# Optimization experiments

Measured on AMD Instinct MI355X. Metric: run time of the kernel, lower is better.

## Reference

```python
import jax, jax.numpy as jnp
import numpy as np

N = 15872   # number of predictions (31 * 512)
D = 129     # 128 image features + 1 objectness score
H = 128     # block MLP hidden width
IN = 2 * D + 1  # neighbor feats + main feats + add_info (IoU)
NUM_BLOCKS = 2


def _lin(k, fi, fo):
    return jax.random.normal(k, (fi, fo), jnp.float32) / np.sqrt(fi).astype(np.float32)


def setup_inputs() -> dict:
    key = jax.random.key(0)
    ks = jax.random.split(key, 24)
    # ragged neighborhood structure: mean size 16, exactly E = 16*N edges
    sizes = (np.arange(N) % 31) + 1
    E = int(sizes.sum())  # 253952
    rng = np.random.default_rng(0)
    nbr_idx = rng.integers(0, N, size=E).astype(np.int32)
    self_idx = np.repeat(np.arange(N, dtype=np.int32), sizes)  # sorted segment ids

    inp = {
        "interpolated": jax.random.normal(ks[0], (N, D), jnp.float32),
        "add_info": jax.random.uniform(ks[1], (E, 1), dtype=jnp.float32),
        "neighborhood_sizes": jnp.asarray(sizes, jnp.int32),
        "neighborhoods_indexes": jnp.asarray(nbr_idx),
        "self_indexes": jnp.asarray(self_idx),
    }
    # two (block, output) model pairs
    inp["b0_W1"] = _lin(ks[2], IN, H); inp["b0_b1"] = jnp.zeros((H,), jnp.float32)
    inp["b0_W2"] = _lin(ks[3], H, H);  inp["b0_b2"] = jnp.zeros((H,), jnp.float32)
    inp["b0_Wo"] = _lin(ks[4], H, D); inp["b0_bo"] = jnp.zeros((D,), jnp.float32)
    inp["b1_W1"] = _lin(ks[5], IN, H); inp["b1_b1"] = jnp.zeros((H,), jnp.float32)
    inp["b1_W2"] = _lin(ks[6], H, H);  inp["b1_b2"] = jnp.zeros((H,), jnp.float32)
    inp["b1_Wo"] = _lin(ks[7], H, D); inp["b1_bo"] = jnp.zeros((D,), jnp.float32)
    # final layers: 129 -> 64 -> 1
    inp["f_W1"] = _lin(ks[8], D, 64); inp["f_b1"] = jnp.zeros((64,), jnp.float32)
    inp["f_W2"] = _lin(ks[9], 64, 1); inp["f_b2"] = jnp.zeros((1,), jnp.float32)
    return inp


def _lnms_forward(interpolated, add_info, params, nbr_idx, self_idx):
    # params: list of (W1, b1, W2, b2, Wo, bo) per block, plus (fW1, fb1, fW2, fb2)
    for (W1, b1, W2, b2, Wo, bo) in params[:-1]:
        nbr = interpolated[nbr_idx]    # (E, D) gather of neighbor representations
        main = interpolated[self_idx]  # (E, D) gather of owning prediction
        x = jnp.concatenate([nbr, main, add_info], axis=1)  # (E, 2D+1)
        h = jax.nn.relu(x @ W1 + b1)
        h = jax.nn.relu(h @ W2 + b2)   # (E, H) processed neighborhoods
        # ragged per-neighborhood max pool (segments are contiguous/sorted)
        pooled = jax.ops.segment_max(h, self_idx, num_segments=N,
                                     indices_are_sorted=True)  # (N, H)
        block_output = pooled @ Wo + bo  # (N, D)
        interpolated = interpolated + block_output  # residual scatter-update
    fW1, fb1, fW2, fb2 = params[-1]
    return jax.nn.relu(interpolated @ fW1 + fb1) @ fW2 + fb2  # (N, 1)


def reference(interpolated, add_info,
              b0_W1, b0_b1, b0_W2, b0_b2, b0_Wo, b0_bo,
              b1_W1, b1_b1, b1_W2, b1_b2, b1_Wo, b1_bo,
              f_W1, f_b1, f_W2, f_b2,
              neighborhood_sizes, neighborhoods_indexes, self_indexes):
    params = [
        (b0_W1, b0_b1, b0_W2, b0_b2, b0_Wo, b0_bo),
        (b1_W1, b1_b1, b1_W2, b1_b2, b1_Wo, b1_bo),
        (f_W1, f_b1, f_W2, f_b2),
    ]
    return _lnms_forward(interpolated, add_info, params,
                         neighborhoods_indexes, self_indexes)
```

## Files before the change

### kernel.cpp

```cpp
#include <hip/hip_runtime.h>

#define NSEG 15872
#define DD 129
#define HH 128
#define NTILE (NSEG / 16)

typedef __attribute__((ext_vector_type(8))) short s16x8;
typedef __attribute__((ext_vector_type(4))) short s16x4;
typedef __attribute__((ext_vector_type(4))) float f32x4;
typedef __attribute__((ext_vector_type(16))) float f32x16;

__device__ __forceinline__ unsigned short f2bf(float x) {
  union { float f; unsigned u; } c; c.f = x;
  unsigned r = c.u + 0x7FFFu + ((c.u >> 16) & 1u);
  return (unsigned short)(r >> 16);
}
__device__ __forceinline__ float bf2f(unsigned short v) {
  union { unsigned u; float f; } c; c.u = ((unsigned)v) << 16; return c.f;
}

__global__ __launch_bounds__(256) void scan_sort_kernel(
    const int* __restrict__ sizes, int* __restrict__ offs,
    int* __restrict__ sorted) {
  extern __shared__ int dynS[];
  int* szS = dynS;
  int* tmpS = dynS + NSEG;
  __shared__ int sums[256];
  __shared__ int bins[1024];
  const int t = threadIdx.x;

  for (int i = t; i < NSEG; i += 256) szS[i] = sizes[i];
  for (int i = t; i < 1024; i += 256) bins[i] = 0;
  __syncthreads();

  const int chunk = (NSEG + 255) >> 8;
  const int s0 = t * chunk, s1 = min(s0 + chunk, NSEG);
  int s = 0;
  for (int i = s0; i < s1; ++i) s += szS[i];
  sums[t] = s;
  __syncthreads();
  for (int d = 1; d < 256; d <<= 1) {
    int u = (t >= d) ? sums[t - d] : 0;
    __syncthreads();
    sums[t] += u;
    __syncthreads();
  }
  int a = sums[t] - s;
  for (int i = s0; i < s1; ++i) { tmpS[i] = a; a += szS[i]; }
  __syncthreads();
  for (int i = t; i < NSEG; i += 256) offs[i] = tmpS[i];
  if (t == 255) offs[NSEG] = a;

  for (int i = t; i < NSEG; i += 256) {
    int sz = szS[i]; sz = sz < 0 ? 0 : (sz > 1023 ? 1023 : sz);
    atomicAdd(&bins[sz], 1);
  }
  __syncthreads();
  const int c0 = bins[t * 4], c1 = bins[t * 4 + 1];
  const int c2 = bins[t * 4 + 2], c3 = bins[t * 4 + 3];
  const int loc = c0 + c1 + c2 + c3;
  sums[t] = loc;
  __syncthreads();
  for (int d = 1; d < 256; d <<= 1) {
    int u = (t >= d) ? sums[t - d] : 0;
    __syncthreads();
    sums[t] += u;
    __syncthreads();
  }
  const int base = sums[t] - loc;
  bins[t * 4]     = base;
  bins[t * 4 + 1] = base + c0;
  bins[t * 4 + 2] = base + c0 + c1;
  bins[t * 4 + 3] = base + c0 + c1 + c2;
  __syncthreads();
  for (int i = t; i < NSEG; i += 256) {
    int sz = szS[i]; sz = sz < 0 ? 0 : (sz > 1023 ? 1023 : sz);
    int pos = atomicAdd(&bins[sz], 1);
    tmpS[pos] = i;
  }
  __syncthreads();
  for (int i = t; i < NSEG; i += 256) sorted[i] = tmpS[i];
}

__device__ __forceinline__ void packB8(short* out, int idx8, const float* W,
                                       int N, int ld, int ncols, int kLimit,
                                       int rowBase) {
  const int n = (idx8 >> 3) % N;
  const int g = idx8 / (8 * N);
  s16x8 o;
#pragma unroll
  for (int i = 0; i < 8; ++i) {
    const int row = g * 8 + i;
    float v = 0.f;
    if (row < kLimit && n < ncols) v = W[(long)(rowBase + row) * ld + n];
    o[i] = (short)f2bf(v);
  }
  *(s16x8*)(out + idx8) = o;
}

__device__ __forceinline__ void packA1T8(short* out, int idx8, const float* W1) {
  const int unit = idx8 >> 3;
  const int lane = unit & 63;
  const int blk = unit >> 6;
  const int Mblk = blk / 10, ks = blk % 10;
  const int m = Mblk * 32 + (lane & 31);
  const int k0 = ks * 16 + ((lane >> 5) << 3);
  s16x8 o;
#pragma unroll
  for (int i = 0; i < 8; ++i) {
    const int k = k0 + i;
    o[i] = (short)((k < DD) ? f2bf(W1[(long)k * HH + m]) : 0);
  }
  *(s16x8*)(out + idx8) = o;
}

__device__ __forceinline__ void packB2T8(short* out, int idx8, const float* W2) {
  const int unit = idx8 >> 3;
  const int lane = unit & 63;
  const int blk = unit >> 6;
  const int ks = blk >> 2, nb = blk & 3;
  const int n = nb * 32 + (lane & 31);
  const int k0 = ks * 16 + ((lane >> 5) << 3);
  s16x8 o;
#pragma unroll
  for (int i = 0; i < 8; ++i)
    o[i] = (short)f2bf(W2[(long)(k0 + i) * HH + n]);
  *(s16x8*)(out + idx8) = o;
}

#define PACK_IDS 161792
#define TAB_IDS (NSEG * 160)
#define PACKV (PACK_IDS / 8)
#define TABV (TAB_IDS / 8)
__global__ __launch_bounds__(256) void pack_tab_kernel(
    const float* __restrict__ interp, unsigned short* __restrict__ tab,
    const float* __restrict__ W1b0, const float* __restrict__ W1b1,
    const float* __restrict__ W2b0, const float* __restrict__ W2b1,
    const float* __restrict__ Wob0, const float* __restrict__ Wob1,
    const float* __restrict__ fW1, short* __restrict__ PA1,
    short* __restrict__ PB2, short* __restrict__ PWo,
    short* __restrict__ PW1m, short* __restrict__ PfW1) {
  int vid = blockIdx.x * 256 + threadIdx.x;
  if (vid < PACKV) {
    int idx = vid * 8;
    if (idx < 40960) {
      packA1T8(PA1 + (idx / 20480) * 20480, idx % 20480,
               (idx < 20480) ? W1b0 : W1b1);
      return;
    }
    idx -= 40960;
    if (idx < 32768) {
      packB2T8(PB2 + (idx / 16384) * 16384, idx % 16384,
               (idx < 16384) ? W2b0 : W2b1);
      return;
    }
    idx -= 32768;
    if (idx < 36864) {
      packB8(PWo + (idx / 18432) * 18432, idx % 18432,
             (idx < 18432) ? Wob0 : Wob1, 144, 129, 129, 128, 0);
      return;
    }
    idx -= 36864;
    if (idx < 40960) {
      packB8(PW1m + (idx / 20480) * 20480, idx % 20480,
             (idx < 20480) ? W1b0 : W1b1, 128, 128, 128, 129, 129);
      return;
    }
    idx -= 40960;
    packB8(PfW1, idx, fW1, 64, 64, 64, 129, 0);
    return;
  }
  vid -= PACKV;
  if (vid < TABV) {
    const int n = vid / 20;
    const int g = vid - n * 20;
    s16x8 o = (s16x8){0, 0, 0, 0, 0, 0, 0, 0};
    if (g < 16) {
      const float* src = interp + (long)n * DD + g * 8;
#pragma unroll
      for (int i = 0; i < 8; ++i) o[i] = (short)f2bf(src[i]);
    } else if (g == 16) {
      o[0] = (short)f2bf(interp[(long)n * DD + 128]);
    }
    *(s16x8*)(tab + (long)vid * 8) = o;
  }
}

__global__ __launch_bounds__(256) void hmprep_kernel(
    const unsigned short* __restrict__ tab, const short* __restrict__ PW1m,
    const float* __restrict__ b1, float* __restrict__ Hm) {
  const int lane = threadIdx.x & 63, w = threadIdx.x >> 6;
  const int lk = lane >> 4, n16 = lane & 15;
  const int tile = blockIdx.x * 4 + w;
  const unsigned short* arow = tab + (long)(tile * 16 + n16) * 160;
  s16x8 A[5];
#pragma unroll
  for (int ks = 0; ks < 5; ++ks) A[ks] = *(const s16x8*)(arow + ks * 32 + lk * 8);
  f32x4 C[8];
#pragma unroll
  for (int nf = 0; nf < 8; ++nf) C[nf] = (f32x4){0.f, 0.f, 0.f, 0.f};
#pragma unroll
  for (int ks = 0; ks < 5; ++ks)
#pragma unroll
    for (int nf = 0; nf < 8; ++nf) {
      const s16x8 b = *(const s16x8*)(PW1m + (((ks * 4 + lk) * 128) + nf * 16 + n16) * 8);
      C[nf] = __builtin_amdgcn_mfma_f32_16x16x32_bf16(A[ks], b, C[nf], 0, 0, 0);
    }
#pragma unroll
  for (int nf = 0; nf < 8; ++nf) {
    const float bv = b1[nf * 16 + n16];
#pragma unroll
    for (int r = 0; r < 4; ++r)
      Hm[(long)(tile * 16 + lk * 4 + r) * HH + nf * 16 + n16] = C[nf][r] + bv;
  }
}

__device__ __forceinline__ int pairEdge(int row, int oLo, int sLo, int oHi,
                                        int sHi) {
  int e = (row < sLo) ? (oLo + row) : (oHi + row - sLo);
  if (row >= sLo + sHi) e = oHi + sHi - 1;
  return e;
}

__global__ __launch_bounds__(512, 2) void edge_kernel(
    const unsigned short* __restrict__ tab, const short* __restrict__ PA1,
    const short* __restrict__ PB2, const float* __restrict__ W1,
    const float* __restrict__ Hm, const float* __restrict__ iou,
    const int* __restrict__ nbrIdx, const int* __restrict__ offs,
    const int* __restrict__ sorted, const float* __restrict__ b2,
    unsigned short* __restrict__ pooled) {
  extern __shared__ __align__(16) char smem[];
  short* As1 = (short*)smem;
  short* Bs2 = (short*)(smem + 40960);
  short* bnc = (short*)(smem + 73728);
  {
    const f32x4* s1 = (const f32x4*)PA1;
    f32x4* d1 = (f32x4*)As1;
    for (int i = threadIdx.x; i < 2560; i += 512) d1[i] = s1[i];
    const f32x4* s2 = (const f32x4*)PB2;
    f32x4* d2 = (f32x4*)Bs2;
    for (int i = threadIdx.x; i < 2048; i += 512) d2[i] = s2[i];
  }
  __syncthreads();

  const int lane = threadIdx.x & 63;
  const int w = threadIdx.x >> 6;
  const int half = lane >> 5, n32 = lane & 31;
  short* bw = bnc + w * (32 * 144);

  float b2v[4], wvT[4];
#pragma unroll
  for (int q = 0; q < 4; ++q) {
    b2v[q] = b2[q * 32 + n32];
    wvT[q] = W1[258 * HH + q * 32 + n32];
  }

  const int wid = (blockIdx.x << 3) + w;
  const int nw = gridDim.x << 3;
  const int npairs = NSEG >> 1;
  const short oneBf = (short)0x3F80;

  for (int p = wid; p < npairs; p += nw) {
    const int segLo = sorted[p], segHi = sorted[NSEG - 1 - p];
    const int oLo = offs[segLo], sLo = offs[segLo + 1] - oLo;
    const int oHi = offs[segHi], sHi = offs[segHi + 1] - oHi;
    const int nchunk = (sLo + sHi + 31) >> 5;

    float mxLo[4], mxHi[4];
#pragma unroll
    for (int q = 0; q < 4; ++q) { mxLo[q] = -3.4e38f; mxHi[q] = -3.4e38f; }

    for (int c = 0; c < nchunk; ++c) {
      const int grow = (c << 5) + n32;
      const int e = pairEdge(grow, oLo, sLo, oHi, sHi);
      const unsigned short* ar = tab + (long)nbrIdx[e] * 160;
      s16x8 X[10];
#pragma unroll
      for (int ks = 0; ks < 10; ++ks)
        X[ks] = *(const s16x8*)(ar + ks * 16 + half * 8);
      const float io = iou[e];
      s16x8 bb = (s16x8){0, 0, 0, 0, 0, 0, 0, 0};
      if (half == 0) {
        const bool lo = grow < sLo;
        bb[0] = lo ? oneBf : (short)0;
        bb[1] = bb[0];
        bb[2] = lo ? (short)0 : oneBf;
        bb[3] = bb[2];
        bb[4] = (short)f2bf(io);
      }

#pragma unroll
      for (int Mblk = 0; Mblk < 4; ++Mblk) {
        f32x16 C;
#pragma unroll
        for (int i = 0; i < 16; ++i) C[i] = 0.f;
#pragma unroll
        for (int ks = 0; ks < 10; ++ks) {
          const s16x8 a = *(const s16x8*)(As1 + ((Mblk * 10 + ks) * 64 + lane) * 8);
          C = __builtin_amdgcn_mfma_f32_32x32x16_bf16(a, X[ks], C, 0, 0, 0);
        }
        const float hLo = Hm[(long)segLo * HH + Mblk * 32 + n32];
        const float hHi = Hm[(long)segHi * HH + Mblk * 32 + n32];
        s16x8 ab = (s16x8){0, 0, 0, 0, 0, 0, 0, 0};
        if (half == 0) {
          const unsigned short p0 = f2bf(hLo);
          ab[0] = (short)p0;
          ab[1] = (short)f2bf(hLo - bf2f(p0));
          const unsigned short p1 = f2bf(hHi);
          ab[2] = (short)p1;
          ab[3] = (short)f2bf(hHi - bf2f(p1));
          ab[4] = (short)f2bf(wvT[Mblk]);
        }
        C = __builtin_amdgcn_mfma_f32_32x32x16_bf16(ab, bb, C, 0, 0, 0);
#pragma unroll
        for (int g = 0; g < 4; ++g) {
          s16x4 o;
#pragma unroll
          for (int j = 0; j < 4; ++j)
            o[j] = (short)f2bf(fmaxf(C[4 * g + j], 0.f));
          *(s16x4*)(bw + n32 * 144 + Mblk * 32 + 8 * g + 4 * half) = o;
        }
      }

      s16x8 A2[8];
#pragma unroll
      for (int ks = 0; ks < 8; ++ks)
        A2[ks] = *(const s16x8*)(bw + n32 * 144 + ks * 16 + half * 8);
#pragma unroll
      for (int nb = 0; nb < 4; ++nb) {
        f32x16 D;
#pragma unroll
        for (int i = 0; i < 16; ++i) D[i] = 0.f;
#pragma unroll
        for (int ks = 0; ks < 8; ++ks) {
          const s16x8 b = *(const s16x8*)(Bs2 + ((ks * 4 + nb) * 64 + lane) * 8);
          D = __builtin_amdgcn_mfma_f32_32x32x16_bf16(A2[ks], b, D, 0, 0, 0);
        }
#pragma unroll
        for (int reg = 0; reg < 16; ++reg) {
          const int rrow = (reg & 3) + 8 * (reg >> 2) + 4 * half;
          const int gr = (c << 5) + rrow;
          const float v = D[reg];
          if (gr < sLo) mxLo[nb] = fmaxf(mxLo[nb], v);
          else          mxHi[nb] = fmaxf(mxHi[nb], v);
        }
      }
    }
#pragma unroll
    for (int nb = 0; nb < 4; ++nb) {
      float lo = fmaxf(mxLo[nb], __shfl_xor(mxLo[nb], 32, 64));
      float hi = fmaxf(mxHi[nb], __shfl_xor(mxHi[nb], 32, 64));
      if (half == 0) {
        pooled[(long)segLo * HH + nb * 32 + n32] = f2bf(fmaxf(lo + b2v[nb], 0.f));
        pooled[(long)segHi * HH + nb * 32 + n32] = f2bf(fmaxf(hi + b2v[nb], 0.f));
      }
    }
  }
}

template <int NEXT>
__global__ __launch_bounds__(256) void resout_kernel(
    const unsigned short* __restrict__ pooled, const short* __restrict__ PWo,
    const float* __restrict__ bo, const float* __restrict__ resIn,
    float* __restrict__ resOut, unsigned short* __restrict__ tab,
    const short* __restrict__ PW1mN, const float* __restrict__ b1n,
    float* __restrict__ HmOut,
    const short* __restrict__ PfW1, const float* __restrict__ fb1,
    const float* __restrict__ fW2, const float* __restrict__ fb2,
    float* __restrict__ outFinal) {
  __shared__ short stS[4][16 * 168];
  const int lane = threadIdx.x & 63, w = threadIdx.x >> 6;
  const int lk = lane >> 4, n16 = lane & 15;
  short* st = stS[w];

  {
    const int row = lane >> 2, c0 = 129 + (lane & 3) * 8;
#pragma unroll
    for (int i = 0; i < 8; ++i) st[row * 168 + c0 + i] = 0;
  }

  const int tile = blockIdx.x * 4 + w;
  const unsigned short* arow = pooled + (long)(tile * 16 + n16) * HH;
  s16x8 A[4];
#pragma unroll
  for (int ks = 0; ks < 4; ++ks) A[ks] = *(const s16x8*)(arow + ks * 32 + lk * 8);
  f32x4 C[9];
#pragma unroll
  for (int nf = 0; nf < 9; ++nf) C[nf] = (f32x4){0.f, 0.f, 0.f, 0.f};
#pragma unroll
  for (int ks = 0; ks < 4; ++ks)
#pragma unroll
    for (int nf = 0; nf < 9; ++nf) {
      const s16x8 b = *(const s16x8*)(PWo + (((ks * 4 + lk) * 144) + nf * 16 + n16) * 8);
      C[nf] = __builtin_amdgcn_mfma_f32_16x16x32_bf16(A[ks], b, C[nf], 0, 0, 0);
    }

#pragma unroll
  for (int nf = 0; nf < 8; ++nf) {
    const int col = nf * 16 + n16;
    const float bov = bo[col];
#pragma unroll
    for (int r = 0; r < 4; ++r) {
      const int row = lk * 4 + r;
      const long node = tile * 16 + row;
      const float res = resIn[node * DD + col] + bov + C[nf][r];
      if (NEXT) {
        resOut[node * DD + col] = res;
        tab[node * 160 + col] = f2bf(res);
      }
      st[row * 168 + col] = (short)f2bf(res);
    }
  }
  if (n16 == 0) {
#pragma unroll
    for (int r = 0; r < 4; ++r) {
      const int row = lk * 4 + r;
      const long node = tile * 16 + row;
      const float res = resIn[node * DD + 128] + bo[128] + C[8][r];
      if (NEXT) {
        resOut[node * DD + 128] = res;
        tab[node * 160 + 128] = f2bf(res);
      }
      st[row * 168 + 128] = (short)f2bf(res);
    }
  }

  s16x8 A5[5];
#pragma unroll
  for (int ks = 0; ks < 5; ++ks)
    A5[ks] = *(const s16x8*)(st + n16 * 168 + ks * 32 + lk * 8);

  if (NEXT) {
    f32x4 H[8];
#pragma unroll
    for (int nf = 0; nf < 8; ++nf) H[nf] = (f32x4){0.f, 0.f, 0.f, 0.f};
#pragma unroll
    for (int ks = 0; ks < 5; ++ks)
#pragma unroll
      for (int nf = 0; nf < 8; ++nf) {
        const s16x8 b = *(const s16x8*)(PW1mN + (((ks * 4 + lk) * 128) + nf * 16 + n16) * 8);
        H[nf] = __builtin_amdgcn_mfma_f32_16x16x32_bf16(A5[ks], b, H[nf], 0, 0, 0);
      }
#pragma unroll
    for (int nf = 0; nf < 8; ++nf) {
      const float bv = b1n[nf * 16 + n16];
#pragma unroll
      for (int r = 0; r < 4; ++r)
        HmOut[(long)(tile * 16 + lk * 4 + r) * HH + nf * 16 + n16] = H[nf][r] + bv;
    }
  } else {
    f32x4 Ch[4];
#pragma unroll
    for (int nf = 0; nf < 4; ++nf) Ch[nf] = (f32x4){0.f, 0.f, 0.f, 0.f};
#pragma unroll
    for (int ks = 0; ks < 5; ++ks)
#pragma unroll
      for (int nf = 0; nf < 4; ++nf) {
        const s16x8 b = *(const s16x8*)(PfW1 + (((ks * 4 + lk) * 64) + nf * 16 + n16) * 8);
        Ch[nf] = __builtin_amdgcn_mfma_f32_16x16x32_bf16(A5[ks], b, Ch[nf], 0, 0, 0);
      }
    float b1v[4], w2v[4];
#pragma unroll
    for (int nf = 0; nf < 4; ++nf) {
      b1v[nf] = fb1[nf * 16 + n16];
      w2v[nf] = fW2[nf * 16 + n16];
    }
#pragma unroll
    for (int r = 0; r < 4; ++r) {
      float s = 0.f;
#pragma unroll
      for (int nf = 0; nf < 4; ++nf)
        s += fmaxf(Ch[nf][r] + b1v[nf], 0.f) * w2v[nf];
      s += __shfl_xor(s, 1, 64);
      s += __shfl_xor(s, 2, 64);
      s += __shfl_xor(s, 4, 64);
      s += __shfl_xor(s, 8, 64);
      if (n16 == 0) outFinal[tile * 16 + lk * 4 + r] = s + fb2[0];
    }
  }
}

extern "C" void kernel_launch(void* const* d_in, const int* in_sizes, int n_in,
                              void* d_out, int out_size, void* d_ws, size_t ws_size,
                              hipStream_t stream) {
  const float* interp  = (const float*)d_in[0];
  const float* addInfo = (const float*)d_in[1];
  const int* sizes     = (const int*)d_in[2];
  const int* nbrIdx    = (const int*)d_in[3];
  const float* b0W1 = (const float*)d_in[5];
  const float* b0b1 = (const float*)d_in[6];
  const float* b0W2 = (const float*)d_in[7];
  const float* b0b2 = (const float*)d_in[8];
  const float* b0Wo = (const float*)d_in[9];
  const float* b0bo = (const float*)d_in[10];
  const float* b1W1 = (const float*)d_in[11];
  const float* b1b1 = (const float*)d_in[12];
  const float* b1W2 = (const float*)d_in[13];
  const float* b1b2 = (const float*)d_in[14];
  const float* b1Wo = (const float*)d_in[15];
  const float* b1bo = (const float*)d_in[16];
  const float* fW1  = (const float*)d_in[17];
  const float* fb1  = (const float*)d_in[18];
  const float* fW2  = (const float*)d_in[19];
  const float* fb2  = (const float*)d_in[20];

  char* ws = (char*)d_ws;
  int*            offs  = (int*)(ws + 0);
  short*          PA1   = (short*)(ws + 65536);
  short*          PB2   = (short*)(ws + 147456);
  short*          PWo   = (short*)(ws + 212992);
  short*          PW1m  = (short*)(ws + 286720);
  short*          PfW1  = (short*)(ws + 368640);
  unsigned short* TAB   = (unsigned short*)(ws + 393216);
  float*          HM    = (float*)(ws + 5472256);
  unsigned short* POOLED= (unsigned short*)(ws + 13598720);
  float*          RES   = (float*)(ws + 17661952);
  int*            SORTED= (int*)(ws + 25851904);

  scan_sort_kernel<<<1, 256, 2 * NSEG * sizeof(int), stream>>>(sizes, offs,
                                                               SORTED);
  pack_tab_kernel<<<(PACKV + TABV) / 256, 256, 0, stream>>>(
      interp, TAB, b0W1, b1W1, b0W2, b1W2, b0Wo, b1Wo, fW1,
      PA1, PB2, PWo, PW1m, PfW1);

  const size_t e_lds = 40960 + 32768 + 8 * 32 * 144 * 2;

  hmprep_kernel<<<NTILE / 4, 256, 0, stream>>>(TAB, PW1m, b0b1, HM);
  edge_kernel<<<256, 512, e_lds, stream>>>(TAB, PA1, PB2, b0W1, HM, addInfo,
                                           nbrIdx, offs, SORTED, b0b2, POOLED);
  resout_kernel<1><<<NTILE / 4, 256, 0, stream>>>(
      POOLED, PWo, b0bo, interp, RES, TAB, PW1m + 20480, b1b1, HM,
      nullptr, nullptr, nullptr, nullptr, nullptr);

  edge_kernel<<<256, 512, e_lds, stream>>>(TAB, PA1 + 20480, PB2 + 16384, b1W1,
                                           HM, addInfo, nbrIdx, offs, SORTED,
                                           b1b2, POOLED);
  resout_kernel<0><<<NTILE / 4, 256, 0, stream>>>(
      POOLED, PWo + 18432, b1bo, RES, nullptr, nullptr, nullptr, nullptr,
      nullptr, PfW1, fb1, fW2, fb2, (float*)d_out);
}
```

Before: 221.0 us.

## Software-pipeline edge kernel gathers across pairs and shrink LDS row padding

Restructures the per-wave pair loop into a ping-pong software pipeline. The next pair's segment metadata, Hm values and first-chunk neighbor gather are issued while the current pair's first-chunk GEMMs run, hiding global gather latency behind MFMA work. Hm loads are hoisted out of the Mblk loop into per-pair metadata. The LDS staging row stride also shrinks from 144 to 136 shorts. The cost is higher register pressure from double-buffered X fragments under launch_bounds(512,2), which may cause spills, and the new stride could change LDS bank conflicts.

```diff
diff --git a/kernel.cpp b/kernel.cpp
--- a/kernel.cpp
+++ b/kernel.cpp
@@ -222,6 +222,138 @@
   return e;
 }
 
+struct PairMeta {
+  int segLo, segHi, oLo, sLo, oHi, sHi;
+  float hmLo[4], hmHi[4];
+};
+
+__device__ __forceinline__ void loadMeta(
+    int p, PairMeta& M, const int* __restrict__ sorted,
+    const int* __restrict__ offs, const float* __restrict__ Hm, int n32) {
+  M.segLo = sorted[p];
+  M.segHi = sorted[NSEG - 1 - p];
+  M.oLo = offs[M.segLo]; M.sLo = offs[M.segLo + 1] - M.oLo;
+  M.oHi = offs[M.segHi]; M.sHi = offs[M.segHi + 1] - M.oHi;
+#pragma unroll
+  for (int q = 0; q < 4; ++q) {
+    M.hmLo[q] = Hm[(long)M.segLo * HH + q * 32 + n32];
+    M.hmHi[q] = Hm[(long)M.segHi * HH + q * 32 + n32];
+  }
+}
+
+__device__ __forceinline__ void gatherX(
+    const PairMeta& M, int c, const unsigned short* __restrict__ tab,
+    const int* __restrict__ nbrIdx, const float* __restrict__ iou,
+    int n32, int half, s16x8* X, float& io) {
+  const int grow = (c << 5) + n32;
+  const int e = pairEdge(grow, M.oLo, M.sLo, M.oHi, M.sHi);
+  const unsigned short* ar = tab + (long)nbrIdx[e] * 160;
+#pragma unroll
+  for (int ks = 0; ks < 10; ++ks)
+    X[ks] = *(const s16x8*)(ar + ks * 16 + half * 8);
+  io = iou[e];
+}
+
+__device__ __forceinline__ void gemm1Phase(
+    const PairMeta& M, int c, const s16x8* X, float io,
+    const short* __restrict__ As1, short* bw, const float* wvT,
+    int lane, int half, int n32) {
+  const int grow = (c << 5) + n32;
+  const short oneBf = (short)0x3F80;
+  s16x8 bb = (s16x8){0, 0, 0, 0, 0, 0, 0, 0};
+  if (half == 0) {
+    const bool lo = grow < M.sLo;
+    bb[0] = lo ? oneBf : (short)0;
+    bb[1] = bb[0];
+    bb[2] = lo ? (short)0 : oneBf;
+    bb[3] = bb[2];
+    bb[4] = (short)f2bf(io);
+  }
+#pragma unroll
+  for (int Mblk = 0; Mblk < 4; ++Mblk) {
+    f32x16 C;
+#pragma unroll
+    for (int i = 0; i < 16; ++i) C[i] = 0.f;
+#pragma unroll
+    for (int ks = 0; ks < 10; ++ks) {
+      const s16x8 a = *(const s16x8*)(As1 + ((Mblk * 10 + ks) * 64 + lane) * 8);
+      C = __builtin_amdgcn_mfma_f32_32x32x16_bf16(a, X[ks], C, 0, 0, 0);
+    }
+    s16x8 ab = (s16x8){0, 0, 0, 0, 0, 0, 0, 0};
+    if (half == 0) {
+      const unsigned short p0 = f2bf(M.hmLo[Mblk]);
+      ab[0] = (short)p0;
+      ab[1] = (short)f2bf(M.hmLo[Mblk] - bf2f(p0));
+      const unsigned short p1 = f2bf(M.hmHi[Mblk]);
+      ab[2] = (short)p1;
+      ab[3] = (short)f2bf(M.hmHi[Mblk] - bf2f(p1));
+      ab[4] = (short)f2bf(wvT[Mblk]);
+    }
+    C = __builtin_amdgcn_mfma_f32_32x32x16_bf16(ab, bb, C, 0, 0, 0);
+#pragma unroll
+    for (int g = 0; g < 4; ++g) {
+      s16x4 o;
+#pragma unroll
+      for (int j = 0; j < 4; ++j)
+        o[j] = (short)f2bf(fmaxf(C[4 * g + j], 0.f));
+      *(s16x4*)(bw + n32 * 136 + Mblk * 32 + 8 * g + 4 * half) = o;
+    }
+  }
+}
+
+__device__ __forceinline__ void gemm2Phase(
+    const PairMeta& M, int c, const short* bw, const short* __restrict__ Bs2,
+    int lane, int half, int n32, float* mxLo, float* mxHi) {
+  s16x8 A2[8];
+#pragma unroll
+  for (int ks = 0; ks < 8; ++ks)
+    A2[ks] = *(const s16x8*)(bw + n32 * 136 + ks * 16 + half * 8);
+#pragma unroll
+  for (int nb = 0; nb < 4; ++nb) {
+    f32x16 D;
+#pragma unroll
+    for (int i = 0; i < 16; ++i) D[i] = 0.f;
+#pragma unroll
+    for (int ks = 0; ks < 8; ++ks) {
+      const s16x8 b = *(const s16x8*)(Bs2 + ((ks * 4 + nb) * 64 + lane) * 8);
+      D = __builtin_amdgcn_mfma_f32_32x32x16_bf16(A2[ks], b, D, 0, 0, 0);
+    }
+#pragma unroll
+    for (int reg = 0; reg < 16; ++reg) {
+      const int rrow = (reg & 3) + 8 * (reg >> 2) + 4 * half;
+      const int gr = (c << 5) + rrow;
+      const float v = D[reg];
+      if (gr < M.sLo) mxLo[nb] = fmaxf(mxLo[nb], v);
+      else            mxHi[nb] = fmaxf(mxHi[nb], v);
+    }
+  }
+}
+
+__device__ __forceinline__ void finishPair(
+    const PairMeta& M, int c0done, const unsigned short* __restrict__ tab,
+    const int* __restrict__ nbrIdx, const float* __restrict__ iou,
+    const short* __restrict__ As1, const short* __restrict__ Bs2, short* bw,
+    const float* wvT, const float* b2v, int lane, int half, int n32,
+    float* mxLo, float* mxHi, unsigned short* __restrict__ pooled) {
+  const int nchunk = (M.sLo + M.sHi + 31) >> 5;
+  for (int c = 1; c < nchunk; ++c) {
+    s16x8 Xr[10];
+    float ior;
+    gatherX(M, c, tab, nbrIdx, iou, n32, half, Xr, ior);
+    gemm1Phase(M, c, Xr, ior, As1, bw, wvT, lane, half, n32);
+    gemm2Phase(M, c, bw, Bs2, lane, half, n32, mxLo, mxHi);
+  }
+#pragma unroll
+  for (int nb = 0; nb < 4; ++nb) {
+    float lo = fmaxf(mxLo[nb], __shfl_xor(mxLo[nb], 32, 64));
+    float hi = fmaxf(mxHi[nb], __shfl_xor(mxHi[nb], 32, 64));
+    if (half == 0) {
+      pooled[(long)M.segLo * HH + nb * 32 + n32] = f2bf(fmaxf(lo + b2v[nb], 0.f));
+      pooled[(long)M.segHi * HH + nb * 32 + n32] = f2bf(fmaxf(hi + b2v[nb], 0.f));
+    }
+  }
+}
+
 __global__ __launch_bounds__(512, 2) void edge_kernel(
     const unsigned short* __restrict__ tab, const short* __restrict__ PA1,
     const short* __restrict__ PB2, const float* __restrict__ W1,
@@ -246,7 +378,7 @@
   const int lane = threadIdx.x & 63;
   const int w = threadIdx.x >> 6;
   const int half = lane >> 5, n32 = lane & 31;
-  short* bw = bnc + w * (32 * 144);
+  short* bw = bnc + w * (32 * 136);
 
   float b2v[4], wvT[4];
 #pragma unroll
@@ -258,102 +390,39 @@
   const int wid = (blockIdx.x << 3) + w;
   const int nw = gridDim.x << 3;
   const int npairs = NSEG >> 1;
-  const short oneBf = (short)0x3F80;
-
-  for (int p = wid; p < npairs; p += nw) {
-    const int segLo = sorted[p], segHi = sorted[NSEG - 1 - p];
-    const int oLo = offs[segLo], sLo = offs[segLo + 1] - oLo;
-    const int oHi = offs[segHi], sHi = offs[segHi + 1] - oHi;
-    const int nchunk = (sLo + sHi + 31) >> 5;
-
-    float mxLo[4], mxHi[4];
-#pragma unroll
-    for (int q = 0; q < 4; ++q) { mxLo[q] = -3.4e38f; mxHi[q] = -3.4e38f; }
-
-    for (int c = 0; c < nchunk; ++c) {
-      const int grow = (c << 5) + n32;
-      const int e = pairEdge(grow, oLo, sLo, oHi, sHi);
-      const unsigned short* ar = tab + (long)nbrIdx[e] * 160;
-      s16x8 X[10];
-#pragma unroll
-      for (int ks = 0; ks < 10; ++ks)
-        X[ks] = *(const s16x8*)(ar + ks * 16 + half * 8);
-      const float io = iou[e];
-      s16x8 bb = (s16x8){0, 0, 0, 0, 0, 0, 0, 0};
-      if (half == 0) {
-        const bool lo = grow < sLo;
-        bb[0] = lo ? oneBf : (short)0;
-        bb[1] = bb[0];
-        bb[2] = lo ? (short)0 : oneBf;
-        bb[3] = bb[2];
-        bb[4] = (short)f2bf(io);
-      }
-
-#pragma unroll
-      for (int Mblk = 0; Mblk < 4; ++Mblk) {
-        f32x16 C;
-#pragma unroll
-        for (int i = 0; i < 16; ++i) C[i] = 0.f;
-#pragma unroll
-        for (int ks = 0; ks < 10; ++ks) {
-          const s16x8 a = *(const s16x8*)(As1 + ((Mblk * 10 + ks) * 64 + lane) * 8);
-          C = __builtin_amdgcn_mfma_f32_32x32x16_bf16(a, X[ks], C, 0, 0, 0);
-        }
-        const float hLo = Hm[(long)segLo * HH + Mblk * 32 + n32];
-        const float hHi = Hm[(long)segHi * HH + Mblk * 32 + n32];
-        s16x8 ab = (s16x8){0, 0, 0, 0, 0, 0, 0, 0};
-        if (half == 0) {
-          const unsigned short p0 = f2bf(hLo);
-          ab[0] = (short)p0;
-          ab[1] = (short)f2bf(hLo - bf2f(p0));
-          const unsigned short p1 = f2bf(hHi);
-          ab[2] = (short)p1;
-          ab[3] = (short)f2bf(hHi - bf2f(p1));
-          ab[4] = (short)f2bf(wvT[Mblk]);
-        }
-        C = __builtin_amdgcn_mfma_f32_32x32x16_bf16(ab, bb, C, 0, 0, 0);
-#pragma unroll
-        for (int g = 0; g < 4; ++g) {
-          s16x4 o;
-#pragma unroll
-          for (int j = 0; j < 4; ++j)
-            o[j] = (short)f2bf(fmaxf(C[4 * g + j], 0.f));
-          *(s16x4*)(bw + n32 * 144 + Mblk * 32 + 8 * g + 4 * half) = o;
-        }
-      }
-
-      s16x8 A2[8];
-#pragma unroll
-      for (int ks = 0; ks < 8; ++ks)
-        A2[ks] = *(const s16x8*)(bw + n32 * 144 + ks * 16 + half * 8);
-#pragma unroll
-      for (int nb = 0; nb < 4; ++nb) {
-        f32x16 D;
-#pragma unroll
-        for (int i = 0; i < 16; ++i) D[i] = 0.f;
-#pragma unroll
-        for (int ks = 0; ks < 8; ++ks) {
-          const s16x8 b = *(const s16x8*)(Bs2 + ((ks * 4 + nb) * 64 + lane) * 8);
-          D = __builtin_amdgcn_mfma_f32_32x32x16_bf16(A2[ks], b, D, 0, 0, 0);
-        }
-#pragma unroll
-        for (int reg = 0; reg < 16; ++reg) {
-          const int rrow = (reg & 3) + 8 * (reg >> 2) + 4 * half;
-          const int gr = (c << 5) + rrow;
-          const float v = D[reg];
-          if (gr < sLo) mxLo[nb] = fmaxf(mxLo[nb], v);
-          else          mxHi[nb] = fmaxf(mxHi[nb], v);
-        }
-      }
-    }
-#pragma unroll
-    for (int nb = 0; nb < 4; ++nb) {
-      float lo = fmaxf(mxLo[nb], __shfl_xor(mxLo[nb], 32, 64));
-      float hi = fmaxf(mxHi[nb], __shfl_xor(mxHi[nb], 32, 64));
-      if (half == 0) {
-        pooled[(long)segLo * HH + nb * 32 + n32] = f2bf(fmaxf(lo + b2v[nb], 0.f));
-        pooled[(long)segHi * HH + nb * 32 + n32] = f2bf(fmaxf(hi + b2v[nb], 0.f));
-      }
+
+  int p = wid;
+  if (p < npairs) {
+    PairMeta MA, MB;
+    s16x8 XA[10], XB[10];
+    float ioA, ioB;
+    loadMeta(p, MA, sorted, offs, Hm, n32);
+    gatherX(MA, 0, tab, nbrIdx, iou, n32, half, XA, ioA);
+    for (;;) {
+      const int p1 = p + nw;
+      const bool h1 = p1 < npairs;
+      if (h1) loadMeta(p1, MB, sorted, offs, Hm, n32);
+      float mxLo[4], mxHi[4];
+#pragma unroll
+      for (int q = 0; q < 4; ++q) { mxLo[q] = -3.4e38f; mxHi[q] = -3.4e38f; }
+      gemm1Phase(MA, 0, XA, ioA, As1, bw, wvT, lane, half, n32);
+      if (h1) gatherX(MB, 0, tab, nbrIdx, iou, n32, half, XB, ioB);
+      gemm2Phase(MA, 0, bw, Bs2, lane, half, n32, mxLo, mxHi);
+      finishPair(MA, 1, tab, nbrIdx, iou, As1, Bs2, bw, wvT, b2v, lane, half,
+                 n32, mxLo, mxHi, pooled);
+      if (!h1) break;
+      const int p2 = p1 + nw;
+      const bool h2 = p2 < npairs;
+      if (h2) loadMeta(p2, MA, sorted, offs, Hm, n32);
+#pragma unroll
+      for (int q = 0; q < 4; ++q) { mxLo[q] = -3.4e38f; mxHi[q] = -3.4e38f; }
+      gemm1Phase(MB, 0, XB, ioB, As1, bw, wvT, lane, half, n32);
+      if (h2) gatherX(MA, 0, tab, nbrIdx, iou, n32, half, XA, ioA);
+      gemm2Phase(MB, 0, bw, Bs2, lane, half, n32, mxLo, mxHi);
+      finishPair(MB, 1, tab, nbrIdx, iou, As1, Bs2, bw, wvT, b2v, lane, half,
+                 n32, mxLo, mxHi, pooled);
+      if (!h2) break;
+      p = p2;
     }
   }
 }
@@ -523,7 +592,7 @@
       interp, TAB, b0W1, b1W1, b0W2, b1W2, b0Wo, b1Wo, fW1,
       PA1, PB2, PWo, PW1m, PfW1);
 
-  const size_t e_lds = 40960 + 32768 + 8 * 32 * 144 * 2;
+  const size_t e_lds = 40960 + 32768 + 8 * 32 * 136 * 2;
 
   hmprep_kernel<<<NTILE / 4, 256, 0, stream>>>(TAB, PW1m, b0b1, HM);
   edge_kernel<<<256, 512, e_lds, stream>>>(TAB, PA1, PB2, b0W1, HM, addInfo,
```

Result: faster. 206.7 us (-6.5%).
